# Optimization experiments

Hardware: AMD Instinct MI355X
Metric: run time of the kernel (lower is better)

## Reference

```python
import jax, jax.numpy as jnp
import numpy as np

EPS = 1e-5  # torch BatchNorm default eps
SLOPE = 0.2  # LeakyReLU negative slope


def bn_apply(h, p):
    # p: (4, C) stacked [gamma, beta, running_mean, running_var]; h channel-last
    g, b, m, v = p[0], p[1], p[2], p[3]
    return (h - m) * (g * jax.lax.rsqrt(v + EPS)) + b


def graph_feature(x, k):
    # x: (B, N, C) -> (B, N, k, 2C) = concat(neighbor - center, center)
    inner = jnp.einsum('bnc,bmc->bnm', x, x)
    sq = jnp.sum(x * x, axis=-1)
    # negative squared pairwise distance (B, N, N)
    pd = 2.0 * inner - sq[:, :, None] - sq[:, None, :]
    idx = jax.lax.top_k(pd, k)[1]  # (B, N, k)
    nbr = jax.vmap(lambda xb, ib: xb[ib])(x, idx)  # (B, N, k, C) gather
    ctr = jnp.broadcast_to(x[:, :, None, :], nbr.shape)
    return jnp.concatenate([nbr - ctr, ctr], axis=-1)


def edge_block(h, w, bnp, k):
    # h: (B, N, C); w: (O, 2C) 1x1 conv weight; returns (B, N, O) after max over k
    f = graph_feature(h, k)
    z = jnp.einsum('bnkc,oc->bnko', f, w)
    z = jax.nn.leaky_relu(bn_apply(z, bnp), SLOPE)
    return jnp.max(z, axis=2)


def setup_inputs() -> dict:
    key = jax.random.key(0)
    ks = jax.random.split(key, 10)
    B, N, K = 16, 1024, 20
    emb, ncls = 1024, 40

    def bnp(c):
        return jnp.stack([jnp.ones(c), jnp.zeros(c), jnp.zeros(c), jnp.ones(c)])

    s = 0.05
    return {
        'x': jax.random.normal(ks[0], (B, 3, N), dtype=jnp.float32),
        'w1': jax.random.normal(ks[1], (64, 6), dtype=jnp.float32) * s,
        'bn1': bnp(64),
        'w2': jax.random.normal(ks[2], (64, 128), dtype=jnp.float32) * s,
        'bn2': bnp(64),
        'w3': jax.random.normal(ks[3], (128, 128), dtype=jnp.float32) * s,
        'bn3': bnp(128),
        'w4': jax.random.normal(ks[4], (256, 256), dtype=jnp.float32) * s,
        'bn4': bnp(256),
        'w5': jax.random.normal(ks[5], (emb, 512), dtype=jnp.float32) * s,
        'bn5': bnp(emb),
        'wl1': jax.random.normal(ks[6], (512, 2 * emb), dtype=jnp.float32) * s,
        'bn6': bnp(512),
        'wl2': jax.random.normal(ks[7], (256, 512), dtype=jnp.float32) * s,
        'bn7': bnp(256),
        'wl3': jax.random.normal(ks[8], (ncls, 256), dtype=jnp.float32) * s,
        'bl3': jax.random.normal(ks[9], (ncls,), dtype=jnp.float32) * s,
        'k': K,
    }


def reference(x, w1, bn1, w2, bn2, w3, bn3, w4, bn4, w5, bn5,
              wl1, bn6, wl2, bn7, wl3, bl3, k):
    # x: (B, 3, N) -> logits (B, num_classes); eval-mode BN, dropout = identity
    h0 = jnp.transpose(x, (0, 2, 1))  # (B, N, 3)
    x1 = edge_block(h0, w1, bn1, k)   # (B, N, 64)
    x2 = edge_block(x1, w2, bn2, k)   # (B, N, 64)
    x3 = edge_block(x2, w3, bn3, k)   # (B, N, 128)
    x4 = edge_block(x3, w4, bn4, k)   # (B, N, 256)
    h = jnp.concatenate([x1, x2, x3, x4], axis=-1)  # (B, N, 512)
    h = jax.nn.leaky_relu(bn_apply(jnp.einsum('bnc,oc->bno', h, w5), bn5), SLOPE)
    p = jnp.concatenate([jnp.max(h, axis=1), jnp.mean(h, axis=1)], axis=-1)  # (B, 2*emb)
    h = jax.nn.leaky_relu(bn_apply(p @ wl1.T, bn6), SLOPE)
    h = jax.nn.leaky_relu(bn_apply(h @ wl2.T, bn7), SLOPE)
    return h @ wl3.T + bl3
```

## Files before the change

kernel.cpp:

```cpp
#include <hip/hip_runtime.h>

#define BB 16
#define NN 1024
#define KNN 20
#define BNEPS 1e-5f

typedef __attribute__((ext_vector_type(8))) short short8;
typedef __attribute__((ext_vector_type(4))) float f32x4;

__device__ __forceinline__ float4 ld4(const float* p){ return *(const float4*)p; }
__device__ __forceinline__ void fma4(float4& a, float s, float4 w){
  a.x = fmaf(s, w.x, a.x); a.y = fmaf(s, w.y, a.y);
  a.z = fmaf(s, w.z, a.z); a.w = fmaf(s, w.w, a.w);
}
__device__ __forceinline__ void max4(float4& a, float4 v){
  a.x = fmaxf(a.x, v.x); a.y = fmaxf(a.y, v.y);
  a.z = fmaxf(a.z, v.z); a.w = fmaxf(a.w, v.w);
}
__device__ __forceinline__ unsigned short f2bf(float f){
  unsigned int u = __float_as_uint(f);
  u = (u + 0x7FFF + ((u >> 16) & 1)) >> 16;
  return (unsigned short)u;
}
__device__ __forceinline__ f32x4 mfma16(short8 a, short8 b, f32x4 c){
  return __builtin_amdgcn_mfma_f32_16x16x32_bf16(a, b, c, 0, 0, 0);
}

__device__ __forceinline__ void top3_build(const float* rp, int kmr,
                                           float& a0, float& a1, float& a2,
                                           int& i0, int& i1, int& i2){
  a0 = -1e30f; a1 = -1e30f; a2 = -1e30f; i0 = 0; i1 = 0; i2 = 0;
#pragma unroll
  for (int r = 0; r < 4; r++){
    float4 t = ld4(rp + r*4);
    float tv[4] = {t.x, t.y, t.z, t.w};
#pragma unroll
    for (int q = 0; q < 4; q++){
      int e = r*4 + q;
      float v = ((kmr >> e) & 1) ? -1e30f : tv[q];
      bool b0 = v > a0, b1 = v > a1, b2 = v > a2;
      a2 = b1 ? a1 : (b2 ? v : a2); i2 = b1 ? i1 : (b2 ? e : i2);
      a1 = b0 ? a0 : (b1 ? v : a1); i1 = b0 ? i0 : (b1 ? e : i1);
      a0 = b0 ? v  : a0;            i0 = b0 ? e : i0;
    }
  }
}

__global__ __launch_bounds__(256) void k_transpose(const float* __restrict__ x, float* __restrict__ xt,
                                                   float* __restrict__ sq){
  int i = blockIdx.x*256 + threadIdx.x;
  if (i >= BB*NN) return;
  int b = i >> 10, n = i & 1023;
  const float* xb = x + (size_t)b*3*NN;
  float4 v;
  v.x = xb[0*NN+n]; v.y = xb[1*NN+n]; v.z = xb[2*NN+n]; v.w = 0.f;
  ((float4*)xt)[i] = v;
  sq[i] = v.x*v.x + v.y*v.y + v.z*v.z;
}

__device__ __forceinline__ void prep_w_dev(int i, const float* w, const float* bnp,
                                           float* wlT, float* dT, float* bias, int Cin, int Cpad, int Cout){
  if (i >= Cpad*Cout) return;
  int c = i / Cout, o = i - c*Cout;
  float s = bnp[o] * rsqrtf(bnp[3*Cout+o] + BNEPS);
  float wl = (c < Cin) ? w[(size_t)o*2*Cin + c] : 0.f;
  float wr = (c < Cin) ? w[(size_t)o*2*Cin + Cin + c] : 0.f;
  wlT[i] = wl * s;
  dT[i]  = (wr - wl) * s;
  if (c == 0) bias[o] = bnp[Cout+o] - bnp[2*Cout+o]*s;
}
__device__ __forceinline__ void prep_wbf_dev(int i, const float* w, const float* bnp,
                                             unsigned short* wlB, unsigned short* dB, float* bias,
                                             int Cin, int Cout){
  if (i >= Cin*Cout) return;
  int o = i / Cin, c = i - o*Cin;
  float s = bnp[o] * rsqrtf(bnp[3*Cout+o] + BNEPS);
  float wl = w[(size_t)o*2*Cin + c] * s;
  float wr = w[(size_t)o*2*Cin + Cin + c] * s;
  wlB[i] = f2bf(wl);
  dB[i]  = f2bf(wr - wl);
  if (c == 0) bias[o] = bnp[Cout+o] - bnp[2*Cout+o]*s;
}

__global__ __launch_bounds__(256) void k_prep_all(const float* __restrict__ w1, const float* __restrict__ bn1,
                                                  const float* __restrict__ w2, const float* __restrict__ bn2,
                                                  const float* __restrict__ w3, const float* __restrict__ bn3,
                                                  const float* __restrict__ w4, const float* __restrict__ bn4,
                                                  const float* __restrict__ w5, const float* __restrict__ bn5,
                                                  float* __restrict__ wlT1, float* __restrict__ dT1, float* __restrict__ bias1,
                                                  unsigned short* __restrict__ wlB2, unsigned short* __restrict__ dB2, float* __restrict__ bias2,
                                                  unsigned short* __restrict__ wlB3, unsigned short* __restrict__ dB3, float* __restrict__ bias3,
                                                  unsigned short* __restrict__ wlB4, unsigned short* __restrict__ dB4, float* __restrict__ bias4,
                                                  unsigned short* __restrict__ w5b, float* __restrict__ b5){
  int bid = blockIdx.x, t = threadIdx.x;
  if (bid < 1){
    prep_w_dev(t, w1, bn1, wlT1, dT1, bias1, 3, 4, 64);
  } else if (bid < 17){
    prep_wbf_dev((bid-1)*256 + t, w2, bn2, wlB2, dB2, bias2, 64, 64);
  } else if (bid < 49){
    prep_wbf_dev((bid-17)*256 + t, w3, bn3, wlB3, dB3, bias3, 64, 128);
  } else if (bid < 177){
    prep_wbf_dev((bid-49)*256 + t, w4, bn4, wlB4, dB4, bias4, 128, 256);
  } else {
    int i = (bid-177)*256 + t;
    int o = i >> 9, c = i & 511;
    float s = bn5[o] * rsqrtf(bn5[3*1024+o] + BNEPS);
    w5b[i] = f2bf(w5[(size_t)o*512 + c] * s);
    if (c == 0) b5[o] = bn5[1024+o] - bn5[2*1024+o]*s;
  }
}

__global__ __launch_bounds__(256) void k_sq(const float* __restrict__ xin, int rs, int Cin, float* __restrict__ sq){
  int i = blockIdx.x*256 + threadIdx.x;
  if (i >= BB*NN) return;
  const float* r = xin + (size_t)i*rs;
  float s = 0.f;
  for (int c = 0; c < Cin; c += 4){
    float4 v = ld4(r + c);
    s += v.x*v.x + v.y*v.y + v.z*v.z + v.w*v.w;
  }
  sq[i] = s;
}

__global__ __launch_bounds__(256) void k_pd(const float* __restrict__ xin, int rs, int Cin, int CT, int lnf4,
                                            const float* __restrict__ sq, float* __restrict__ pd){
  extern __shared__ float lds[];
  const int pitch = CT + 4;
  float* As = lds;
  float* Bs = lds + 64*pitch;
  const int b = blockIdx.y;
  int t = blockIdx.x, ti = 0;
  while (t >= 16 - ti){ t -= (16 - ti); ti++; }
  const int tj = ti + t;
  const int n0 = ti*64, m0 = tj*64;
  const int tid = threadIdx.x;
  const int tx = tid & 15, ty = tid >> 4;
  const float* xb = xin + (size_t)b*NN*rs;
  float acc[4][4];
#pragma unroll
  for (int i = 0; i < 4; i++)
#pragma unroll
    for (int j = 0; j < 4; j++) acc[i][j] = 0.f;

  const int nf4 = CT >> 2;
  for (int c0 = 0; c0 < Cin; c0 += CT){
    for (int e = tid; e < 64*nf4; e += 256){
      int r = e >> lnf4, cc = (e & (nf4-1))*4;
      *(float4*)(As + r*pitch + cc) = ld4(xb + (size_t)(n0+r)*rs + c0 + cc);
      *(float4*)(Bs + r*pitch + cc) = ld4(xb + (size_t)(m0+r)*rs + c0 + cc);
    }
    __syncthreads();
    for (int c = 0; c < CT; c += 4){
      float4 a[4], bv[4];
#pragma unroll
      for (int i = 0; i < 4; i++) a[i]  = ld4(As + (ty+16*i)*pitch + c);
#pragma unroll
      for (int j = 0; j < 4; j++) bv[j] = ld4(Bs + (tx+16*j)*pitch + c);
#pragma unroll
      for (int i = 0; i < 4; i++)
#pragma unroll
        for (int j = 0; j < 4; j++){
          acc[i][j] = fmaf(a[i].x, bv[j].x, acc[i][j]);
          acc[i][j] = fmaf(a[i].y, bv[j].y, acc[i][j]);
          acc[i][j] = fmaf(a[i].z, bv[j].z, acc[i][j]);
          acc[i][j] = fmaf(a[i].w, bv[j].w, acc[i][j]);
        }
    }
    __syncthreads();
  }

#pragma unroll
  for (int i = 0; i < 4; i++){
    int n = n0 + ty + 16*i;
#pragma unroll
    for (int j = 0; j < 4; j++){
      int m = m0 + tx + 16*j;
      pd[((size_t)b*NN + n)*NN + m] = 2.f*acc[i][j] - sq[b*NN + m];
    }
  }

  if (ti != tj){
    const int PT = 68;
    float* Ltr = lds;
    float sqn[4];
#pragma unroll
    for (int i = 0; i < 4; i++) sqn[i] = sq[b*NN + n0 + ty + 16*i];
#pragma unroll
    for (int i = 0; i < 4; i++)
#pragma unroll
      for (int j = 0; j < 4; j++)
        Ltr[(tx + 16*j)*PT + ty + 16*i] = 2.f*acc[i][j] - sqn[i];
    __syncthreads();
    for (int e = tid; e < 64*16; e += 256){
      int r = e >> 4, c4 = (e & 15)*4;
      *(float4*)(pd + ((size_t)b*NN + m0 + r)*NN + n0 + c4) = *(float4*)(Ltr + r*PT + c4);
    }
  }
}

__global__ __launch_bounds__(256) void k_topk(const float* __restrict__ pd, int* __restrict__ idxOut){
  int w = threadIdx.x >> 6, lane = threadIdx.x & 63;
  int bn0 = (blockIdx.x*4 + w)*2;
  const float* row0 = pd + (size_t)bn0*NN + lane*16;
  const float* row1 = row0 + NN;

  float c0v[2], c1v[2], c2v[2];
  int   c0i[2], c1i[2], c2i[2];
  int   km[2] = {0, 0};
  top3_build(row0, 0, c0v[0], c1v[0], c2v[0], c0i[0], c1i[0], c2i[0]);
  top3_build(row1, 0, c0v[1], c1v[1], c2v[1], c0i[1], c1i[1], c2i[1]);

  int* out0 = idxOut + (size_t)bn0*KNN;
  int* out1 = out0 + KNN;
  for (int it = 0; it < KNN; it++){
    float g0 = c0v[0], g1 = c0v[1];
#pragma unroll
    for (int s = 1; s < 64; s <<= 1){
      g0 = fmaxf(g0, __shfl_xor(g0, s));
      g1 = fmaxf(g1, __shfl_xor(g1, s));
    }
    int o0 = __ffsll(__ballot(c0v[0] == g0)) - 1;
    int o1 = __ffsll(__ballot(c0v[1] == g1)) - 1;
    bool u0 = (lane == o0), u1 = (lane == o1);
    if (u0) out0[it] = lane*16 + c0i[0];
    if (u1) out1[it] = lane*16 + c0i[1];
    km[0] |= u0 ? (1 << c0i[0]) : 0;
    km[1] |= u1 ? (1 << c0i[1]) : 0;
    c0v[0] = u0 ? c1v[0] : c0v[0];  c0i[0] = u0 ? c1i[0] : c0i[0];
    c1v[0] = u0 ? c2v[0] : c1v[0];  c1i[0] = u0 ? c2i[0] : c1i[0];
    c2v[0] = u0 ? -1e30f : c2v[0];
    c0v[1] = u1 ? c1v[1] : c0v[1];  c0i[1] = u1 ? c1i[1] : c0i[1];
    c1v[1] = u1 ? c2v[1] : c1v[1];  c1i[1] = u1 ? c2i[1] : c1i[1];
    c2v[1] = u1 ? -1e30f : c2v[1];
    if (it < KNN-1){
      bool rp0 = (c0v[0] == -1e30f) && (km[0] != 0xFFFF);
      bool rp1 = (c0v[1] == -1e30f) && (km[1] != 0xFFFF);
      if (__ballot(rp0 || rp1)){
        if (rp0) top3_build(row0, km[0], c0v[0], c1v[0], c2v[0], c0i[0], c1i[0], c2i[0]);
        if (rp1) top3_build(row1, km[1], c0v[1], c1v[1], c2v[1], c0i[1], c1i[1], c2i[1]);
      }
    }
  }
}

__global__ __launch_bounds__(256) void k_uv1(const float* __restrict__ xt,
                                             const float* __restrict__ wlT, const float* __restrict__ dT,
                                             float* __restrict__ Z){
  int t = blockIdx.x*256 + threadIdx.x;
  int n = t >> 5, q = t & 31;
  float4 xv = ld4(xt + (size_t)n*4);
  const float* wp = (q < 16) ? (wlT + q*4) : (dT + (q-16)*4);
  float4 a = make_float4(0.f,0.f,0.f,0.f);
  fma4(a, xv.x, ld4(wp + 0*64));
  fma4(a, xv.y, ld4(wp + 1*64));
  fma4(a, xv.z, ld4(wp + 2*64));
  fma4(a, xv.w, ld4(wp + 3*64));
  *(float4*)(Z + (size_t)n*128 + q*4) = a;
}

template<int K>
__global__ __launch_bounds__(256) void k_uv(const unsigned short* __restrict__ hbi,
                                            const unsigned short* __restrict__ wB,
                                            float* __restrict__ Z, int ldz){
  __shared__ char sm[20480];
  char* As = sm; char* Bs = sm + 10240;
  const int tid = threadIdx.x, lane = tid & 63, w = tid >> 6;
  const int l15 = lane & 15, quad = lane >> 4;
  const int n0 = blockIdx.x*128, r0 = blockIdx.y*128;

  f32x4 acc[2][8];
  f32x4 zero = {0.f,0.f,0.f,0.f};
#pragma unroll
  for (int i = 0; i < 2; i++)
#pragma unroll
    for (int j = 0; j < 8; j++) acc[i][j] = zero;

  for (int k0 = 0; k0 < K; k0 += 32){
#pragma unroll
    for (int i = 0; i < 2; i++){
      int e = tid + i*256;
      int r = e >> 2, sg = e & 3;
      *(float4*)(As + r*80 + sg*16) = *(const float4*)(hbi + ((size_t)(r0+r))*512 + k0 + sg*8);
      *(float4*)(Bs + r*80 + sg*16) = *(const float4*)(wB  + ((size_t)(n0+r))*K   + k0 + sg*8);
    }
    __syncthreads();
    short8 af0 = *(short8*)(As + (w*32 + l15)*80 + quad*16);
    short8 af1 = *(short8*)(As + (w*32 + 16 + l15)*80 + quad*16);
#pragma unroll
    for (int ns = 0; ns < 8; ns++){
      short8 bf = *(short8*)(Bs + (ns*16 + l15)*80 + quad*16);
      acc[0][ns] = mfma16(af0, bf, acc[0][ns]);
      acc[1][ns] = mfma16(af1, bf, acc[1][ns]);
    }
    __syncthreads();
  }

#pragma unroll
  for (int ms = 0; ms < 2; ms++){
#pragma unroll
    for (int ns = 0; ns < 8; ns++){
      f32x4 a = acc[ms][ns];
      int row = r0 + w*32 + ms*16 + quad*4;
      int col = n0 + ns*16 + l15;
#pragma unroll
      for (int r = 0; r < 4; r++)
        Z[(size_t)(row+r)*ldz + col] = a[r];
    }
  }
}

template<int COUT, int P, bool WF32>
__global__ __launch_bounds__(256) void k_gmax(const float* __restrict__ Z,
                                              const float* __restrict__ bias,
                                              const int* __restrict__ knn_idx,
                                              float* __restrict__ hf,
                                              unsigned short* __restrict__ hbo){
  constexpr int QPP = COUT/4;
  __shared__ int idxS[P*KNN];
  const int tid = threadIdx.x;
  const int p0 = blockIdx.x * P;
  for (int t = tid; t < P*KNN; t += 256) idxS[t] = knn_idx[(size_t)p0*KNN + t];
  __syncthreads();

  const int p = tid / QPP, q = tid - p*QPP;
  const int base = p0 & ~1023;
  const int ldz = 2*COUT;
  const float* Zq = Z + q*4;

  float4 m = make_float4(-1e30f,-1e30f,-1e30f,-1e30f);
#pragma unroll
  for (int j = 0; j < KNN; j++){
    int mr = idxS[p*KNN + j];
    max4(m, ld4(Zq + (size_t)(base + mr)*ldz));
  }
  float4 ctr = ld4(Z + (size_t)(p0+p)*ldz + COUT + q*4);
  float4 bs  = ld4(bias + q*4);
  float4 y;
  y.x = m.x + ctr.x + bs.x; y.x = fmaxf(y.x, 0.2f*y.x);
  y.y = m.y + ctr.y + bs.y; y.y = fmaxf(y.y, 0.2f*y.y);
  y.z = m.z + ctr.z + bs.z; y.z = fmaxf(y.z, 0.2f*y.z);
  y.w = m.w + ctr.w + bs.w; y.w = fmaxf(y.w, 0.2f*y.w);

  size_t pi = (size_t)(p0 + p);
  if (WF32) *(float4*)(hf + pi*256 + q*4) = y;
  ushort4 hv; hv.x = f2bf(y.x); hv.y = f2bf(y.y); hv.z = f2bf(y.z); hv.w = f2bf(y.w);
  *(ushort4*)(hbo + pi*512 + q*4) = hv;
}

__global__ __launch_bounds__(256) void k_conv5m(const unsigned short* __restrict__ hb,
                                                const unsigned short* __restrict__ w5b,
                                                const float* __restrict__ b5,
                                                float* __restrict__ pmax, float* __restrict__ psum){
  __shared__ char sm[20480 + 4096];
  char* As = sm; char* Bs = sm + 10240;
  float* red = (float*)(sm + 20480);
  const int tid = threadIdx.x, lane = tid & 63, w = tid >> 6;
  const int l15 = lane & 15, quad = lane >> 4;
  const int n0 = blockIdx.x*128, r0 = blockIdx.y*128;

  f32x4 acc[2][8];
  f32x4 zero = {0.f,0.f,0.f,0.f};
#pragma unroll
  for (int i = 0; i < 2; i++)
#pragma unroll
    for (int j = 0; j < 8; j++) acc[i][j] = zero;

  for (int k0 = 0; k0 < 512; k0 += 32){
#pragma unroll
    for (int i = 0; i < 2; i++){
      int e = tid + i*256;
      int r = e >> 2, sg = e & 3;
      *(float4*)(As + r*80 + sg*16) = *(const float4*)(hb  + ((size_t)(r0+r))*512 + k0 + sg*8);
      *(float4*)(Bs + r*80 + sg*16) = *(const float4*)(w5b + ((size_t)(n0+r))*512 + k0 + sg*8);
    }
    __syncthreads();
    short8 af0 = *(short8*)(As + (w*32 + l15)*80 + quad*16);
    short8 af1 = *(short8*)(As + (w*32 + 16 + l15)*80 + quad*16);
#pragma unroll
    for (int ns = 0; ns < 8; ns++){
      short8 bf = *(short8*)(Bs + (ns*16 + l15)*80 + quad*16);
      acc[0][ns] = mfma16(af0, bf, acc[0][ns]);
      acc[1][ns] = mfma16(af1, bf, acc[1][ns]);
    }
    __syncthreads();
  }

#pragma unroll
  for (int ns = 0; ns < 8; ns++){
    float bv = b5[n0 + ns*16 + l15];
    float mx = -1e30f, sum = 0.f;
#pragma unroll
    for (int ms = 0; ms < 2; ms++){
      float* a = (float*)&acc[ms][ns];
#pragma unroll
      for (int r = 0; r < 4; r++){
        float v = a[r] + bv; v = fmaxf(v, 0.2f*v);
        mx = fmaxf(mx, v); sum += v;
      }
    }
    for (int s = 16; s < 64; s <<= 1){
      mx = fmaxf(mx, __shfl_xor(mx, s));
      sum += __shfl_xor(sum, s);
    }
    if (quad == 0){ red[(w*8 + ns)*16 + l15] = mx; red[512 + (w*8 + ns)*16 + l15] = sum; }
  }
  __syncthreads();
  if (tid < 128){
    int ns = tid >> 4, ci = tid & 15;
    float mx = -1e30f, sum = 0.f;
#pragma unroll
    for (int w2 = 0; w2 < 4; w2++){
      mx = fmaxf(mx, red[(w2*8 + ns)*16 + ci]);
      sum += red[512 + (w2*8 + ns)*16 + ci];
    }
    pmax[(size_t)blockIdx.y*1024 + n0 + tid] = mx;
    psum[(size_t)blockIdx.y*1024 + n0 + tid] = sum;
  }
}

__global__ __launch_bounds__(256) void k_fc1(const float* __restrict__ pmax, const float* __restrict__ psum,
                                             const float* __restrict__ wl1, const float* __restrict__ bn6,
                                             float* __restrict__ h1){
  __shared__ float pS[2048];
  const int b = blockIdx.y, t = threadIdx.x;
  for (int f = t; f < 512; f += 256){
    float4 r;
    if (f < 256){
      r = ld4(pmax + (size_t)(b*8)*1024 + f*4);
#pragma unroll
      for (int ch = 1; ch < 8; ch++) max4(r, ld4(pmax + (size_t)(b*8+ch)*1024 + f*4));
    } else {
      int o = (f-256)*4;
      r = ld4(psum + (size_t)(b*8)*1024 + o);
#pragma unroll
      for (int ch = 1; ch < 8; ch++){
        float4 s = ld4(psum + (size_t)(b*8+ch)*1024 + o);
        r.x += s.x; r.y += s.y; r.z += s.z; r.w += s.w;
      }
      r.x *= (1.f/1024.f); r.y *= (1.f/1024.f); r.z *= (1.f/1024.f); r.w *= (1.f/1024.f);
    }
    ((float4*)pS)[f] = r;
  }
  __syncthreads();
  const int ol = t >> 4, ch = t & 15;
  const int o = blockIdx.x*16 + ol;
  const float* wr = wl1 + (size_t)o*2048;
  float acc = 0.f;
#pragma unroll
  for (int j = 0; j < 32; j++){
    int c = ch*4 + j*64;
    float4 wv = ld4(wr + c);
    acc += pS[c]*wv.x + pS[c+1]*wv.y + pS[c+2]*wv.z + pS[c+3]*wv.w;
  }
#pragma unroll
  for (int s = 1; s < 16; s <<= 1) acc += __shfl_xor(acc, s);
  if (ch == 0){
    float s = bn6[o] * rsqrtf(bn6[3*512+o] + BNEPS);
    float y = (acc - bn6[2*512+o])*s + bn6[512+o];
    h1[(size_t)b*512 + o] = fmaxf(y, 0.2f*y);
  }
}

__global__ __launch_bounds__(256) void k_fc2(const float* __restrict__ h1,
                                             const float* __restrict__ wl2, const float* __restrict__ bn7,
                                             float* __restrict__ h2){
  __shared__ float hS[512];
  const int b = blockIdx.y, t = threadIdx.x;
  if (t < 128) ((float4*)hS)[t] = ((const float4*)(h1 + (size_t)b*512))[t];
  __syncthreads();
  const int ol = t >> 4, ch = t & 15;
  const int o = blockIdx.x*16 + ol;
  const float* wr = wl2 + (size_t)o*512;
  float acc = 0.f;
#pragma unroll
  for (int j = 0; j < 8; j++){
    int c = ch*4 + j*64;
    float4 wv = ld4(wr + c);
    acc += hS[c]*wv.x + hS[c+1]*wv.y + hS[c+2]*wv.z + hS[c+3]*wv.w;
  }
#pragma unroll
  for (int s = 1; s < 16; s <<= 1) acc += __shfl_xor(acc, s);
  if (ch == 0){
    float s = bn7[o] * rsqrtf(bn7[3*256+o] + BNEPS);
    float y = (acc - bn7[2*256+o])*s + bn7[256+o];
    h2[(size_t)b*256 + o] = fmaxf(y, 0.2f*y);
  }
}

__global__ __launch_bounds__(64) void k_fc3(const float* __restrict__ h2,
                                            const float* __restrict__ wl3, const float* __restrict__ bl3,
                                            float* __restrict__ out){
  const int o = blockIdx.x, b = blockIdx.y, lane = threadIdx.x;
  float4 wv = ld4(wl3 + (size_t)o*256 + lane*4);
  float4 hv = ld4(h2 + (size_t)b*256 + lane*4);
  float acc = hv.x*wv.x + hv.y*wv.y + hv.z*wv.z + hv.w*wv.w;
#pragma unroll
  for (int s = 1; s < 64; s <<= 1) acc += __shfl_xor(acc, s);
  if (lane == 0) out[(size_t)b*40 + o] = acc + bl3[o];
}

extern "C" void kernel_launch(void* const* d_in, const int* in_sizes, int n_in,
                              void* d_out, int out_size, void* d_ws, size_t ws_size,
                              hipStream_t stream) {
  (void)in_sizes; (void)n_in; (void)out_size; (void)ws_size;
  const float* x   = (const float*)d_in[0];
  const float* w1  = (const float*)d_in[1];
  const float* bn1 = (const float*)d_in[2];
  const float* w2  = (const float*)d_in[3];
  const float* bn2 = (const float*)d_in[4];
  const float* w3  = (const float*)d_in[5];
  const float* bn3 = (const float*)d_in[6];
  const float* w4  = (const float*)d_in[7];
  const float* bn4 = (const float*)d_in[8];
  const float* w5  = (const float*)d_in[9];
  const float* bn5 = (const float*)d_in[10];
  const float* wl1 = (const float*)d_in[11];
  const float* bn6 = (const float*)d_in[12];
  const float* wl2 = (const float*)d_in[13];
  const float* bn7 = (const float*)d_in[14];
  const float* wl3 = (const float*)d_in[15];
  const float* bl3 = (const float*)d_in[16];
  float* out = (float*)d_out;

  float* ws    = (float*)d_ws;
  float* xt    = ws;
  float* sqb   = xt + 65536;
  int*   idxb  = (int*)(sqb + 16384);
  float* pd    = (float*)(idxb + 327680);
  float* h     = pd + 16777216;
  float* wlT1  = h + 4194304;
  float* dT1   = wlT1 + 256;
  float* bias1 = dT1 + 256;
  float* bias2 = bias1 + 64;
  float* bias3 = bias2 + 64;
  float* bias4 = bias3 + 128;
  float* b5    = bias4 + 256;
  float* pmax  = b5 + 1024;
  float* psum  = pmax + 131072;
  float* pool  = psum + 131072;
  float* h1b   = pool + 32768;
  float* h2b   = h1b + 8192;
  unsigned short* hb   = (unsigned short*)(h2b + 4096);
  unsigned short* wlB2 = hb + (size_t)16384*512;
  unsigned short* dB2  = wlB2 + 4096;
  unsigned short* wlB3 = dB2 + 4096;
  unsigned short* dB3  = wlB3 + 8192;
  unsigned short* wlB4 = dB3 + 8192;
  unsigned short* dB4  = wlB4 + 32768;
  unsigned short* w5b  = dB4 + 32768;
  float* Z = pd;

  k_transpose<<<64, 256, 0, stream>>>(x, xt, sqb);
  k_prep_all<<<2225, 256, 0, stream>>>(w1, bn1, w2, bn2, w3, bn3, w4, bn4, w5, bn5,
                                       wlT1, dT1, bias1, wlB2, dB2, bias2,
                                       wlB3, dB3, bias3, wlB4, dB4, bias4, w5b, b5);

  const size_t PD_LDS64 = 34816;
  const size_t PD_LDS4  = 17408;

  k_pd<<<dim3(136,16), 256, PD_LDS4, stream>>>(xt, 4, 4, 4, 0, sqb, pd);
  k_topk<<<2048, 256, 0, stream>>>(pd, idxb);
  k_uv1<<<2048, 256, 0, stream>>>(xt, wlT1, dT1, Z);
  k_gmax<64,16,true><<<1024, 256, 0, stream>>>(Z, bias1, idxb, h, hb);

  k_sq<<<64, 256, 0, stream>>>(h, 256, 64, sqb);
  k_pd<<<dim3(136,16), 256, PD_LDS64, stream>>>(h, 256, 64, 64, 4, sqb, pd);
  k_topk<<<2048, 256, 0, stream>>>(pd, idxb);
  k_uv<64><<<dim3(1,128), 256, 0, stream>>>(hb, wlB2, Z, 128);
  k_gmax<64,16,true><<<1024, 256, 0, stream>>>(Z, bias2, idxb, h + 64, hb + 64);

  k_sq<<<64, 256, 0, stream>>>(h + 64, 256, 64, sqb);
  k_pd<<<dim3(136,16), 256, PD_LDS64, stream>>>(h + 64, 256, 64, 64, 4, sqb, pd);
  k_topk<<<2048, 256, 0, stream>>>(pd, idxb);
  k_uv<64><<<dim3(2,128), 256, 0, stream>>>(hb + 64, wlB3, Z, 256);
  k_gmax<128,8,true><<<2048, 256, 0, stream>>>(Z, bias3, idxb, h + 128, hb + 128);

  k_sq<<<64, 256, 0, stream>>>(h + 128, 256, 128, sqb);
  k_pd<<<dim3(136,16), 256, PD_LDS64, stream>>>(h + 128, 256, 128, 64, 4, sqb, pd);
  k_topk<<<2048, 256, 0, stream>>>(pd, idxb);
  k_uv<128><<<dim3(4,128), 256, 0, stream>>>(hb + 128, wlB4, Z, 512);
  k_gmax<256,4,false><<<4096, 256, 0, stream>>>(Z, bias4, idxb, nullptr, hb + 256);

  k_conv5m<<<dim3(8,128), 256, 0, stream>>>(hb, w5b, b5, pmax, psum);
  k_fc1<<<dim3(32,16), 256, 0, stream>>>(pmax, psum, wl1, bn6, h1b);
  k_fc2<<<dim3(16,16), 256, 0, stream>>>(h1b, wl2, bn7, h2b);
  k_fc3<<<dim3(40,16), 64, 0, stream>>>(h2b, wl3, bl3, out);
}
```

Before: 462.8 us.

## Compute pairwise distances with split-bf16 MFMA instead of fp32 FMA

```diff
diff --git a/kernel.cpp b/kernel.cpp
--- a/kernel.cpp
+++ b/kernel.cpp
@@ -21,6 +21,9 @@
   unsigned int u = __float_as_uint(f);
   u = (u + 0x7FFF + ((u >> 16) & 1)) >> 16;
   return (unsigned short)u;
+}
+__device__ __forceinline__ float bf2f(unsigned short u){
+  return __uint_as_float(((unsigned int)u) << 16);
 }
 __device__ __forceinline__ f32x4 mfma16(short8 a, short8 b, f32x4 c){
   return __builtin_amdgcn_mfma_f32_16x16x32_bf16(a, b, c, 0, 0, 0);
@@ -47,6 +50,7 @@
 }
 
 __global__ __launch_bounds__(256) void k_transpose(const float* __restrict__ x, float* __restrict__ xt,
+                                                   unsigned short* __restrict__ hlo,
                                                    float* __restrict__ sq){
   int i = blockIdx.x*256 + threadIdx.x;
   if (i >= BB*NN) return;
@@ -55,7 +59,20 @@
   float4 v;
   v.x = xb[0*NN+n]; v.y = xb[1*NN+n]; v.z = xb[2*NN+n]; v.w = 0.f;
   ((float4*)xt)[i] = v;
-  sq[i] = v.x*v.x + v.y*v.y + v.z*v.z;
+  unsigned short hx = f2bf(v.x), hy = f2bf(v.y), hz = f2bf(v.z);
+  float rx = v.x - bf2f(hx), ry = v.y - bf2f(hy), rz = v.z - bf2f(hz);
+  unsigned short lx = f2bf(rx), ly = f2bf(ry), lz = f2bf(rz);
+  float ex = bf2f(hx)+bf2f(lx), ey = bf2f(hy)+bf2f(ly), ez = bf2f(hz)+bf2f(lz);
+  sq[i] = ex*ex + ey*ey + ez*ez;
+  ushort4 h4 = {hx, hy, hz, 0};
+  ushort4 l4 = {lx, ly, lz, 0};
+  ushort4 z4 = {0, 0, 0, 0};
+  unsigned short* pa = hlo + (size_t)i*512 + 256;
+  unsigned short* pb = hlo + (size_t)i*512 + 288;
+  *(ushort4*)(pa+0) = h4; *(ushort4*)(pa+4) = l4; *(ushort4*)(pa+8) = h4;
+  *(ushort4*)(pb+0) = h4; *(ushort4*)(pb+4) = h4; *(ushort4*)(pb+8) = l4;
+#pragma unroll
+  for (int s = 12; s < 32; s += 4){ *(ushort4*)(pa+s) = z4; *(ushort4*)(pb+s) = z4; }
 }
 
 __device__ __forceinline__ void prep_w_dev(int i, const float* w, const float* bnp,
@@ -110,90 +127,133 @@
   }
 }
 
-__global__ __launch_bounds__(256) void k_sq(const float* __restrict__ xin, int rs, int Cin, float* __restrict__ sq){
+template<int CC>
+__global__ __launch_bounds__(256) void k_sqb(const unsigned short* __restrict__ hb,
+                                             const unsigned short* __restrict__ hlo,
+                                             float* __restrict__ sq){
   int i = blockIdx.x*256 + threadIdx.x;
   if (i >= BB*NN) return;
-  const float* r = xin + (size_t)i*rs;
+  const unsigned short* ph = hb  + (size_t)i*512;
+  const unsigned short* pl = hlo + (size_t)i*512;
   float s = 0.f;
-  for (int c = 0; c < Cin; c += 4){
-    float4 v = ld4(r + c);
-    s += v.x*v.x + v.y*v.y + v.z*v.z + v.w*v.w;
+#pragma unroll
+  for (int c = 0; c < CC; c += 4){
+    ushort4 a = *(const ushort4*)(ph + c);
+    ushort4 b = *(const ushort4*)(pl + c);
+    float v0 = bf2f(a.x)+bf2f(b.x), v1 = bf2f(a.y)+bf2f(b.y);
+    float v2 = bf2f(a.z)+bf2f(b.z), v3 = bf2f(a.w)+bf2f(b.w);
+    s += v0*v0 + v1*v1 + v2*v2 + v3*v3;
   }
   sq[i] = s;
 }
 
-__global__ __launch_bounds__(256) void k_pd(const float* __restrict__ xin, int rs, int Cin, int CT, int lnf4,
-                                            const float* __restrict__ sq, float* __restrict__ pd){
-  extern __shared__ float lds[];
-  const int pitch = CT + 4;
-  float* As = lds;
-  float* Bs = lds + 64*pitch;
-  const int b = blockIdx.y;
-  int t = blockIdx.x, ti = 0;
-  while (t >= 16 - ti){ t -= (16 - ti); ti++; }
-  const int tj = ti + t;
-  const int n0 = ti*64, m0 = tj*64;
-  const int tid = threadIdx.x;
-  const int tx = tid & 15, ty = tid >> 4;
-  const float* xb = xin + (size_t)b*NN*rs;
-  float acc[4][4];
-#pragma unroll
-  for (int i = 0; i < 4; i++)
-#pragma unroll
-    for (int j = 0; j < 4; j++) acc[i][j] = 0.f;
-
-  const int nf4 = CT >> 2;
-  for (int c0 = 0; c0 < Cin; c0 += CT){
-    for (int e = tid; e < 64*nf4; e += 256){
-      int r = e >> lnf4, cc = (e & (nf4-1))*4;
-      *(float4*)(As + r*pitch + cc) = ld4(xb + (size_t)(n0+r)*rs + c0 + cc);
-      *(float4*)(Bs + r*pitch + cc) = ld4(xb + (size_t)(m0+r)*rs + c0 + cc);
+template<int CC>
+__global__ __launch_bounds__(256) void k_pdm(const unsigned short* __restrict__ hbi,
+                                             const unsigned short* __restrict__ hlo,
+                                             const float* __restrict__ sq,
+                                             float* __restrict__ pd){
+  __shared__ char sm[20480];
+  char* As = sm; char* Bs = sm + 10240;
+  const int tid = threadIdx.x, lane = tid & 63, w = tid >> 6;
+  const int l15 = lane & 15, quad = lane >> 4;
+  const int b = blockIdx.y >> 3, rt = blockIdx.y & 7;
+  const size_t ar0 = (size_t)b*NN + rt*128;
+  const size_t br0 = (size_t)b*NN + blockIdx.x*128;
+
+  f32x4 acc[2][8];
+  f32x4 zero = {0.f,0.f,0.f,0.f};
+#pragma unroll
+  for (int i = 0; i < 2; i++)
+#pragma unroll
+    for (int j = 0; j < 8; j++) acc[i][j] = zero;
+
+  for (int k0 = 0; k0 < 3*CC; k0 += 32){
+    int seg = k0 / CC, off = k0 - seg*CC;
+    const unsigned short* Ap = (seg == 1) ? hlo : hbi;
+    const unsigned short* Bp = (seg == 2) ? hlo : hbi;
+#pragma unroll
+    for (int i = 0; i < 2; i++){
+      int e = tid + i*256;
+      int r = e >> 2, sg = e & 3;
+      *(float4*)(As + r*80 + sg*16) = *(const float4*)(Ap + (ar0+r)*512 + off + sg*8);
+      *(float4*)(Bs + r*80 + sg*16) = *(const float4*)(Bp + (br0+r)*512 + off + sg*8);
     }
     __syncthreads();
-    for (int c = 0; c < CT; c += 4){
-      float4 a[4], bv[4];
-#pragma unroll
-      for (int i = 0; i < 4; i++) a[i]  = ld4(As + (ty+16*i)*pitch + c);
-#pragma unroll
-      for (int j = 0; j < 4; j++) bv[j] = ld4(Bs + (tx+16*j)*pitch + c);
-#pragma unroll
-      for (int i = 0; i < 4; i++)
-#pragma unroll
-        for (int j = 0; j < 4; j++){
-          acc[i][j] = fmaf(a[i].x, bv[j].x, acc[i][j]);
-          acc[i][j] = fmaf(a[i].y, bv[j].y, acc[i][j]);
-          acc[i][j] = fmaf(a[i].z, bv[j].z, acc[i][j]);
-          acc[i][j] = fmaf(a[i].w, bv[j].w, acc[i][j]);
-        }
+    short8 af0 = *(short8*)(As + (w*32 + l15)*80 + quad*16);
+    short8 af1 = *(short8*)(As + (w*32 + 16 + l15)*80 + quad*16);
+#pragma unroll
+    for (int ns = 0; ns < 8; ns++){
+      short8 bf = *(short8*)(Bs + (ns*16 + l15)*80 + quad*16);
+      acc[0][ns] = mfma16(af0, bf, acc[0][ns]);
+      acc[1][ns] = mfma16(af1, bf, acc[1][ns]);
     }
     __syncthreads();
   }
 
-#pragma unroll
-  for (int i = 0; i < 4; i++){
-    int n = n0 + ty + 16*i;
-#pragma unroll
-    for (int j = 0; j < 4; j++){
-      int m = m0 + tx + 16*j;
-      pd[((size_t)b*NN + n)*NN + m] = 2.f*acc[i][j] - sq[b*NN + m];
-    }
-  }
-
-  if (ti != tj){
-    const int PT = 68;
-    float* Ltr = lds;
-    float sqn[4];
-#pragma unroll
-    for (int i = 0; i < 4; i++) sqn[i] = sq[b*NN + n0 + ty + 16*i];
-#pragma unroll
-    for (int i = 0; i < 4; i++)
-#pragma unroll
-      for (int j = 0; j < 4; j++)
-        Ltr[(tx + 16*j)*PT + ty + 16*i] = 2.f*acc[i][j] - sqn[i];
-    __syncthreads();
-    for (int e = tid; e < 64*16; e += 256){
-      int r = e >> 4, c4 = (e & 15)*4;
-      *(float4*)(pd + ((size_t)b*NN + m0 + r)*NN + n0 + c4) = *(float4*)(Ltr + r*PT + c4);
+  const int colb = blockIdx.x*128;
+#pragma unroll
+  for (int ms = 0; ms < 2; ms++){
+#pragma unroll
+    for (int ns = 0; ns < 8; ns++){
+      f32x4 a = acc[ms][ns];
+      float sqv = sq[br0 + ns*16 + l15];
+      int row = (int)ar0 + w*32 + ms*16 + quad*4;
+      int col = colb + ns*16 + l15;
+#pragma unroll
+      for (int r = 0; r < 4; r++)
+        pd[(size_t)(row+r)*NN + col] = 2.f*a[r] - sqv;
+    }
+  }
+}
+
+__global__ __launch_bounds__(256) void k_pdm1(const unsigned short* __restrict__ hlo,
+                                              const float* __restrict__ sq,
+                                              float* __restrict__ pd){
+  __shared__ char sm[20480];
+  char* As = sm; char* Bs = sm + 10240;
+  const int tid = threadIdx.x, lane = tid & 63, w = tid >> 6;
+  const int l15 = lane & 15, quad = lane >> 4;
+  const int b = blockIdx.y >> 3, rt = blockIdx.y & 7;
+  const size_t ar0 = (size_t)b*NN + rt*128;
+  const size_t br0 = (size_t)b*NN + blockIdx.x*128;
+
+#pragma unroll
+  for (int i = 0; i < 2; i++){
+    int e = tid + i*256;
+    int r = e >> 2, sg = e & 3;
+    *(float4*)(As + r*80 + sg*16) = *(const float4*)(hlo + (ar0+r)*512 + 256 + sg*8);
+    *(float4*)(Bs + r*80 + sg*16) = *(const float4*)(hlo + (br0+r)*512 + 288 + sg*8);
+  }
+  __syncthreads();
+
+  f32x4 acc[2][8];
+  f32x4 zero = {0.f,0.f,0.f,0.f};
+#pragma unroll
+  for (int i = 0; i < 2; i++)
+#pragma unroll
+    for (int j = 0; j < 8; j++) acc[i][j] = zero;
+
+  short8 af0 = *(short8*)(As + (w*32 + l15)*80 + quad*16);
+  short8 af1 = *(short8*)(As + (w*32 + 16 + l15)*80 + quad*16);
+#pragma unroll
+  for (int ns = 0; ns < 8; ns++){
+    short8 bf = *(short8*)(Bs + (ns*16 + l15)*80 + quad*16);
+    acc[0][ns] = mfma16(af0, bf, acc[0][ns]);
+    acc[1][ns] = mfma16(af1, bf, acc[1][ns]);
+  }
+
+  const int colb = blockIdx.x*128;
+#pragma unroll
+  for (int ms = 0; ms < 2; ms++){
+#pragma unroll
+    for (int ns = 0; ns < 8; ns++){
+      f32x4 a = acc[ms][ns];
+      float sqv = sq[br0 + ns*16 + l15];
+      int row = (int)ar0 + w*32 + ms*16 + quad*4;
+      int col = colb + ns*16 + l15;
+#pragma unroll
+      for (int r = 0; r < 4; r++)
+        pd[(size_t)(row+r)*NN + col] = 2.f*a[r] - sqv;
     }
   }
 }
@@ -309,12 +369,12 @@
   }
 }
 
-template<int COUT, int P, bool WF32>
+template<int COUT, int P, bool WLO>
 __global__ __launch_bounds__(256) void k_gmax(const float* __restrict__ Z,
                                               const float* __restrict__ bias,
                                               const int* __restrict__ knn_idx,
-                                              float* __restrict__ hf,
-                                              unsigned short* __restrict__ hbo){
+                                              unsigned short* __restrict__ hbo,
+                                              unsigned short* __restrict__ hloo){
   constexpr int QPP = COUT/4;
   __shared__ int idxS[P*KNN];
   const int tid = threadIdx.x;
@@ -342,9 +402,14 @@
   y.w = m.w + ctr.w + bs.w; y.w = fmaxf(y.w, 0.2f*y.w);
 
   size_t pi = (size_t)(p0 + p);
-  if (WF32) *(float4*)(hf + pi*256 + q*4) = y;
   ushort4 hv; hv.x = f2bf(y.x); hv.y = f2bf(y.y); hv.z = f2bf(y.z); hv.w = f2bf(y.w);
   *(ushort4*)(hbo + pi*512 + q*4) = hv;
+  if (WLO){
+    ushort4 lv;
+    lv.x = f2bf(y.x - bf2f(hv.x)); lv.y = f2bf(y.y - bf2f(hv.y));
+    lv.z = f2bf(y.z - bf2f(hv.z)); lv.w = f2bf(y.w - bf2f(hv.w));
+    *(ushort4*)(hloo + pi*512 + q*4) = lv;
+  }
 }
 
 __global__ __launch_bounds__(256) void k_conv5m(const unsigned short* __restrict__ hb,
@@ -527,8 +592,8 @@
   float* sqb   = xt + 65536;
   int*   idxb  = (int*)(sqb + 16384);
   float* pd    = (float*)(idxb + 327680);
-  float* h     = pd + 16777216;
-  float* wlT1  = h + 4194304;
+  unsigned short* hlo = (unsigned short*)(pd + 16777216);
+  float* wlT1  = (float*)(hlo + 8388608);
   float* dT1   = wlT1 + 256;
   float* bias1 = dT1 + 256;
   float* bias2 = bias1 + 64;
@@ -550,36 +615,33 @@
   unsigned short* w5b  = dB4 + 32768;
   float* Z = pd;
 
-  k_transpose<<<64, 256, 0, stream>>>(x, xt, sqb);
+  k_transpose<<<64, 256, 0, stream>>>(x, xt, hlo, sqb);
   k_prep_all<<<2225, 256, 0, stream>>>(w1, bn1, w2, bn2, w3, bn3, w4, bn4, w5, bn5,
                                        wlT1, dT1, bias1, wlB2, dB2, bias2,
                                        wlB3, dB3, bias3, wlB4, dB4, bias4, w5b, b5);
 
-  const size_t PD_LDS64 = 34816;
-  const size_t PD_LDS4  = 17408;
-
-  k_pd<<<dim3(136,16), 256, PD_LDS4, stream>>>(xt, 4, 4, 4, 0, sqb, pd);
+  k_pdm1<<<dim3(8,128), 256, 0, stream>>>(hlo, sqb, pd);
   k_topk<<<2048, 256, 0, stream>>>(pd, idxb);
   k_uv1<<<2048, 256, 0, stream>>>(xt, wlT1, dT1, Z);
-  k_gmax<64,16,true><<<1024, 256, 0, stream>>>(Z, bias1, idxb, h, hb);
-
-  k_sq<<<64, 256, 0, stream>>>(h, 256, 64, sqb);
-  k_pd<<<dim3(136,16), 256, PD_LDS64, stream>>>(h, 256, 64, 64, 4, sqb, pd);
+  k_gmax<64,16,true><<<1024, 256, 0, stream>>>(Z, bias1, idxb, hb, hlo);
+
+  k_sqb<64><<<64, 256, 0, stream>>>(hb, hlo, sqb);
+  k_pdm<64><<<dim3(8,128), 256, 0, stream>>>(hb, hlo, sqb, pd);
   k_topk<<<2048, 256, 0, stream>>>(pd, idxb);
   k_uv<64><<<dim3(1,128), 256, 0, stream>>>(hb, wlB2, Z, 128);
-  k_gmax<64,16,true><<<1024, 256, 0, stream>>>(Z, bias2, idxb, h + 64, hb + 64);
-
-  k_sq<<<64, 256, 0, stream>>>(h + 64, 256, 64, sqb);
-  k_pd<<<dim3(136,16), 256, PD_LDS64, stream>>>(h + 64, 256, 64, 64, 4, sqb, pd);
+  k_gmax<64,16,true><<<1024, 256, 0, stream>>>(Z, bias2, idxb, hb + 64, hlo + 64);
+
+  k_sqb<64><<<64, 256, 0, stream>>>(hb + 64, hlo + 64, sqb);
+  k_pdm<64><<<dim3(8,128), 256, 0, stream>>>(hb + 64, hlo + 64, sqb, pd);
   k_topk<<<2048, 256, 0, stream>>>(pd, idxb);
   k_uv<64><<<dim3(2,128), 256, 0, stream>>>(hb + 64, wlB3, Z, 256);
-  k_gmax<128,8,true><<<2048, 256, 0, stream>>>(Z, bias3, idxb, h + 128, hb + 128);
-
-  k_sq<<<64, 256, 0, stream>>>(h + 128, 256, 128, sqb);
-  k_pd<<<dim3(136,16), 256, PD_LDS64, stream>>>(h + 128, 256, 128, 64, 4, sqb, pd);
+  k_gmax<128,8,true><<<2048, 256, 0, stream>>>(Z, bias3, idxb, hb + 128, hlo + 128);
+
+  k_sqb<128><<<64, 256, 0, stream>>>(hb + 128, hlo + 128, sqb);
+  k_pdm<128><<<dim3(8,128), 256, 0, stream>>>(hb + 128, hlo + 128, sqb, pd);
   k_topk<<<2048, 256, 0, stream>>>(pd, idxb);
   k_uv<128><<<dim3(4,128), 256, 0, stream>>>(hb + 128, wlB4, Z, 512);
-  k_gmax<256,4,false><<<4096, 256, 0, stream>>>(Z, bias4, idxb, nullptr, hb + 256);
+  k_gmax<256,4,false><<<4096, 256, 0, stream>>>(Z, bias4, idxb, hb + 256, nullptr);
 
   k_conv5m<<<dim3(8,128), 256, 0, stream>>>(hb, w5b, b5, pmax, psum);
   k_fc1<<<dim3(32,16), 256, 0, stream>>>(pmax, psum, wl1, bn6, h1b);
```

New measurement: 458.5 us. About the same (-0.9%).
